# Performance work log

Hardware: AMD Instinct MI355X
Metric: run time of the kernel (lower is better)

Reference implementation:

```python
import jax, jax.numpy as jnp
import numpy as np

N_QUBITS = 8
N_LAYERS = 2
BATCH = 16384
DIM = 2 ** N_QUBITS

# PauliZ sign table: Z[q, idx] = +1 if bit q of idx is 0 else -1 (qubit 0 = MSB,
# matching state axis ordering below).
_bits = (np.arange(DIM)[:, None] >> (N_QUBITS - 1 - np.arange(N_QUBITS))) & 1
Z_SIGNS = jnp.asarray((1 - 2 * _bits).T.astype(np.float32))  # (n_qubits, 2^n)


def _apply_1q(state, gates, q):
    """Apply batched single-qubit gate. state: (B,)+(2,)*n complex, gates: (B,2,2)."""
    s = jnp.moveaxis(state, 1 + q, -1)
    s = jnp.einsum('nab,...b->...a', gates, s.reshape(gates.shape[0], -1, 2).reshape(s.shape))
    # the einsum above: gates (B,2,2) broadcast over the intermediate axes
    return jnp.moveaxis(s, -1, 1 + q)


def _apply_1q_batched(state, gates, q):
    s = jnp.moveaxis(state, 1 + q, -1)          # (B, ..., 2)
    s = jnp.einsum('nab,n...b->n...a', gates, s)
    return jnp.moveaxis(s, -1, 1 + q)


def _apply_cnot(state, c, t):
    s = jnp.moveaxis(state, (1 + c, 1 + t), (-2, -1))  # (..., 2_ctrl, 2_tgt)
    s = jnp.concatenate([s[..., :1, :], s[..., 1:, ::-1]], axis=-2)  # flip target where ctrl=1
    return jnp.moveaxis(s, (-2, -1), (1 + c, 1 + t))


def _rx_gate(theta):
    """Batched RX(theta): (B,) -> (B,2,2) complex."""
    c = jnp.cos(theta / 2)
    s = -1j * jnp.sin(theta / 2)
    return jnp.stack([jnp.stack([c + 0j, s], -1), jnp.stack([s, c + 0j], -1)], -2)


def _rot_gate(phi, theta, omega):
    """PennyLane Rot(phi,theta,omega) = RZ(omega) RY(theta) RZ(phi). Batched (B,)->(B,2,2)."""
    c = jnp.cos(theta / 2)
    s = jnp.sin(theta / 2)
    ep = jnp.exp(-0.5j * (phi + omega))  # e^{-i(phi+omega)/2}
    em = jnp.exp(0.5j * (phi - omega))   # e^{ i(phi-omega)/2}
    m00 = ep * c
    m01 = -em * s
    m10 = jnp.conj(em) * s
    m11 = jnp.conj(ep) * c
    return jnp.stack([jnp.stack([m00, m01], -1), jnp.stack([m10, m11], -1)], -2)


def _circuit(inputs, hidden):
    B = inputs.shape[0]
    n = N_QUBITS
    state = jnp.zeros((B,) + (2,) * n, jnp.complex64)
    state = state.at[(slice(None),) + (0,) * n].set(1.0 + 0j)
    # AngleEmbedding: RX(inputs[:, q]) on each wire q
    for q in range(n):
        state = _apply_1q_batched(state, _rx_gate(inputs[:, q]), q)
    # n_layers calls of StronglyEntanglingLayers, each with 1 layer of weights
    for l in range(N_LAYERS):
        w = hidden[:, l, 0]  # (B, n_qubits, 3)
        for q in range(n):
            state = _apply_1q_batched(state, _rot_gate(w[:, q, 0], w[:, q, 1], w[:, q, 2]), q)
        for q in range(n):  # CNOT ring, range r = 1
            state = _apply_cnot(state, q, (q + 1) % n)
    probs = jnp.abs(state.reshape(B, DIM)) ** 2          # (B, 2^n)
    expvals = probs @ Z_SIGNS.T                          # (B, n_qubits) <Z_q>
    return jnp.tanh(expvals)


def setup_inputs() -> dict:
    key = jax.random.key(0)
    k1, k2 = jax.random.split(key)
    inputs = jax.random.normal(k1, (BATCH, N_QUBITS), dtype=jnp.float32)
    hidden = jax.random.normal(k2, (BATCH, N_LAYERS, 1, N_QUBITS, 3), dtype=jnp.float32)
    return {"inputs": inputs, "hidden": hidden}


def reference(inputs, hidden):
    h = _circuit(inputs, hidden)
    return (h, h)
```

## Files before the change

### kernel.cpp

```cpp
#include <hip/hip_runtime.h>
#include <math.h>


#define DEVINL __device__ __forceinline__

DEVINL void fast_sincos_half(float x, float& s, float& c) {
    const float r = x * 0.07957747154594767f;
    s = __builtin_amdgcn_sinf(r);
    c = __builtin_amdgcn_cosf(r);
}

DEVINL float fast_tanh(float x) {
    const float t = __builtin_amdgcn_exp2f(x * 2.8853900817779268f);
    return 1.0f - 2.0f * __builtin_amdgcn_rcpf(t + 1.0f);
}

DEVINL void cmul(float ar, float ai, float br, float bi, float& cr, float& ci) {
    cr = ar*br - ai*bi;
    ci = ar*bi + ai*br;
}

template<int CTRL>
DEVINL float dpp_perm(float x) {
    return __int_as_float(__builtin_amdgcn_update_dpp(
        __float_as_int(x), __float_as_int(x), CTRL, 0xF, 0xF, false));
}

DEVINL void qubit_vec(float x, float phi, float theta, float omega,
                      float& v0r, float& v0i, float& v1r, float& v1i)
{
    float s, c;   fast_sincos_half(x, s, c);
    float st, ct; fast_sincos_half(theta, st, ct);
    float sa, ca; fast_sincos_half(phi + omega, sa, ca);
    float sb, cb; fast_sincos_half(phi - omega, sb, cb);
    const float A = c*ct, B = s*st, C = c*st, D = s*ct;
    v0r = ca*A - sb*B;
    v0i = cb*B - sa*A;
    v1r = cb*C + sa*D;
    v1i = -(sb*C + ca*D);
}

template<int KM>
DEVINL void ry_k(float (&ar)[16], float (&ai)[16], float c, float s) {
    #pragma unroll
    for (int k0 = 0; k0 < 16; ++k0) {
        if (k0 & KM) continue;
        const int k1 = k0 | KM;
        const float lr = ar[k0], li = ai[k0], hr = ar[k1], hi = ai[k1];
        ar[k0] = c*lr - s*hr;  ai[k0] = c*li - s*hi;
        ar[k1] = s*lr + c*hr;  ai[k1] = s*li + c*hi;
    }
}

template<int CTRL>
DEVINL void ry_lane(float (&ar)[16], float (&ai)[16], float c, float seff) {
    #pragma unroll
    for (int k = 0; k < 16; ++k) {
        const float pr = dpp_perm<CTRL>(ar[k]);
        const float pi = dpp_perm<CTRL>(ai[k]);
        ar[k] = c*ar[k] + seff*pr;
        ai[k] = c*ai[k] + seff*pi;
    }
}

__global__ __launch_bounds__(256, 4)
void qcirc_kernel(const float* __restrict__ inputs,
                  const float* __restrict__ hidden,
                  float* __restrict__ out, int B)
{
    const int t  = threadIdx.x;
    const int e  = blockIdx.x * 16 + (t >> 4);
    const int sl = t & 15;
    if (e >= B) return;

    const int sl0 = sl & 1, sl1 = (sl >> 1) & 1, sl2 = (sl >> 2) & 1, sl3 = (sl >> 3) & 1;
    const int p01 = sl0 ^ sl1;

    float inv[8], hv[48];
    {
        const float4* ip = (const float4*)(inputs + (size_t)e * 8);
        ((float4*)inv)[0] = ip[0];
        ((float4*)inv)[1] = ip[1];
        const float4* hp = (const float4*)(hidden + (size_t)e * 48);
        #pragma unroll
        for (int j = 0; j < 12; ++j) ((float4*)hv)[j] = hp[j];
    }

    float vr[8][2], vi[8][2];
    #pragma unroll
    for (int q = 0; q < 8; ++q)
        qubit_vec(inv[q], hv[q*3], hv[q*3+1], hv[q*3+2],
                  vr[q][0], vi[q][0], vr[q][1], vi[q][1]);

    const float w0r0 = p01 ? vr[0][1] : vr[0][0], w0i0 = p01 ? vi[0][1] : vi[0][0];
    const float w0r1 = p01 ? vr[0][0] : vr[0][1], w0i1 = p01 ? vi[0][0] : vi[0][1];
    const float w1r0 = p01 ? vr[1][1] : vr[1][0], w1i0 = p01 ? vi[1][1] : vi[1][0];
    const float w1r1 = p01 ? vr[1][0] : vr[1][1], w1i1 = p01 ? vi[1][0] : vi[1][1];
    const float w4r0 = sl3 ? vr[4][1] : vr[4][0], w4i0 = sl3 ? vi[4][1] : vi[4][0];
    const float w4r1 = sl3 ? vr[4][0] : vr[4][1], w4i1 = sl3 ? vi[4][0] : vi[4][1];

    float Lr, Li;
    {
        const int s6 = sl1 ^ sl3, s7 = sl0 ^ sl2;
        const float ar5 = sl2 ? vr[5][1] : vr[5][0], ai5 = sl2 ? vi[5][1] : vi[5][0];
        const float ar6 = s6  ? vr[6][1] : vr[6][0], ai6 = s6  ? vi[6][1] : vi[6][0];
        const float ar7 = s7  ? vr[7][1] : vr[7][0], ai7 = s7  ? vi[7][1] : vi[7][0];
        float tr, ti;
        cmul(ar5, ai5, ar6, ai6, tr, ti);
        cmul(tr, ti, ar7, ai7, Lr, Li);
    }

    float KAr[4], KAi[4];
    #pragma unroll
    for (int j = 0; j < 4; ++j) {
        const int k3 = j >> 1, k2 = j & 1, x = k3 ^ k2;
        const float f0r = k3 ? w0r1 : w0r0, f0i = k3 ? w0i1 : w0i0;
        const float f1r = x  ? w1r1 : w1r0, f1i = x  ? w1i1 : w1i0;
        float tr, ti;
        cmul(f0r, f0i, f1r, f1i, tr, ti);
        cmul(tr, ti, Lr, Li, KAr[j], KAi[j]);
    }
    float KCr[4], KCi[4];
    #pragma unroll
    for (int m = 0; m < 4; ++m) {
        const int k1 = m >> 1, k0 = m & 1, x = k0 ^ k1;
        const float f4r = k0 ? w4r1 : w4r0, f4i = k0 ? w4i1 : w4i0;
        cmul(vr[3][x], vi[3][x], f4r, f4i, KCr[m], KCi[m]);
    }
    float K8r[8], K8i[8];
    #pragma unroll
    for (int m = 0; m < 8; ++m) {
        const int k2 = m >> 2, k1 = (m >> 1) & 1, x = k1 ^ k2;
        cmul(vr[2][x], vi[2][x], KCr[m & 3], KCi[m & 3], K8r[m], K8i[m]);
    }

    const float REV2 = 0.07957747154594767f;
    float h[8];
    #pragma unroll
    for (int p = 0; p < 8; ++p) h[p] = hv[24 + p*3] * REV2;
    const float lam = (sl3        ? h[4] : -h[4]) + ((sl3^sl2) ? h[5] : -h[5])
                    + ((sl2^sl1)  ? h[6] : -h[6]) + ((sl1^sl0) ? h[7] : -h[7]);
    float Aang[4];
    Aang[0] = lam - h[0] - h[1];
    Aang[1] = lam - h[0] + h[1];
    Aang[2] = lam + h[0] - h[1];
    Aang[3] = lam + h[0] + h[1];
    const float Bs = h[2] + h[3], Bd = h[2] - h[3];

    float ar[16], ai[16];
    #pragma unroll
    for (int k = 0; k < 16; ++k) {
        const int j = k >> 2, m = k & 7, mm = k & 3;
        const float ang = Aang[j] + (mm == 0 ? -Bs : mm == 1 ? -Bd : mm == 2 ? Bd : Bs);
        const float cr = __builtin_amdgcn_cosf(ang);
        const float ci = __builtin_amdgcn_sinf(ang);
        float tr, ti;
        cmul(KAr[j], KAi[j], K8r[m], K8i[m], tr, ti);
        cmul(tr, ti, cr, ci, ar[k], ai[k]);
    }

    float s2[8], c2[8];
    #pragma unroll
    for (int p = 0; p < 8; ++p) fast_sincos_half(hv[24 + p*3 + 1], s2[p], c2[p]);

    ry_k<8>(ar, ai, c2[0], s2[0]);
    ry_k<4>(ar, ai, c2[1], s2[1]);
    ry_k<2>(ar, ai, c2[2], s2[2]);
    ry_k<1>(ar, ai, c2[3], s2[3]);

    const float e4 = sl3        ? s2[4] : -s2[4];
    const float e5 = (sl3^sl2)  ? s2[5] : -s2[5];
    const float e6 = (sl2^sl1)  ? s2[6] : -s2[6];
    const float e7 = (sl1^sl0)  ? s2[7] : -s2[7];
    ry_lane<0x140>(ar, ai, c2[4], e4);
    ry_lane<0x141>(ar, ai, c2[5], e5);
    ry_lane<0x1B> (ar, ai, c2[6], e6);
    ry_lane<0xB1> (ar, ai, c2[7], e7);

    float P[16];
    #pragma unroll
    for (int k = 0; k < 16; ++k) P[k] = ar[k]*ar[k] + ai[k]*ai[k];

    float S0[4], S1[4], S3[4];
    #pragma unroll
    for (int j = 0; j < 4; ++j) {
        const float p00 = P[j*4+0], p01v = P[j*4+1], p10 = P[j*4+2], p11 = P[j*4+3];
        const float u = p00 + p01v, w = p10 + p11;
        const float d0 = p00 - p01v, d1 = p10 - p11;
        S0[j] = u + w;
        S1[j] = u - w;
        S3[j] = d0 - d1;
    }
    float VC = S0[0] - S0[1] - S0[2] + S0[3];
    float VE = S1[0] - S1[1] - S1[2] + S1[3];
    float VF = S3[0] - S3[1] - S3[2] + S3[3];
    float V7 = S3[0] - S3[1] + S3[2] - S3[3];

    {
        const float g1 = (sl & 1) ? -1.f : 1.f;
        V7 = fmaf(g1, V7, dpp_perm<0xB1>(V7));
        VC = fmaf(g1, VC, dpp_perm<0xB1>(VC));
        VE = fmaf(g1, VE, dpp_perm<0xB1>(VE));
        VF = fmaf(g1, VF, dpp_perm<0xB1>(VF));
        const float g2 = (sl & 2) ? -1.f : 1.f;
        V7 = fmaf(g2, V7, dpp_perm<0x4E>(V7));
        VC = fmaf(g2, VC, dpp_perm<0x4E>(VC));
        VE = fmaf(g2, VE, dpp_perm<0x4E>(VE));
        VF = fmaf(g2, VF, dpp_perm<0x4E>(VF));
        const float g4 = (sl & 4) ? -1.f : 1.f;
        V7 = fmaf(g4, V7, __shfl_xor(V7, 4, 64));
        VC = fmaf(g4, VC, __shfl_xor(VC, 4, 64));
        VE = fmaf(g4, VE, __shfl_xor(VE, 4, 64));
        VF = fmaf(g4, VF, __shfl_xor(VF, 4, 64));
        const float g8 = (sl & 8) ? -1.f : 1.f;
        V7 = fmaf(g8, V7, __shfl_xor(V7, 8, 64));
        VC = fmaf(g8, VC, __shfl_xor(VC, 8, 64));
        VE = fmaf(g8, VE, __shfl_xor(VE, 8, 64));
        VF = fmaf(g8, VF, __shfl_xor(VF, 8, 64));
    }

    const int gb = (t & 63) & 48;
    const float B7 = __shfl(V7, gb + 1, 64);
    const float BC = __shfl(VC, gb, 64);
    const float BE = __shfl(VE, gb, 64);
    const int fidx = (sl >= 4) ? (128 >> sl) : 0;
    const float BF = __shfl(VF, gb + fidx, 64);
    const float rsel = (sl == 0) ? B7 : (sl == 1) ? BC : (sl == 2) ? BE : BF;
    const float hres = fast_tanh(rsel);
    if (sl < 8) {
        const size_t obase = (size_t)e * 8;
        const size_t half  = (size_t)B * 8;
        out[obase + sl]        = hres;
        out[half + obase + sl] = hres;
    }
}

extern "C" void kernel_launch(void* const* d_in, const int* in_sizes, int n_in,
                              void* d_out, int out_size, void* d_ws, size_t ws_size,
                              hipStream_t stream)
{
    const float* inputs = (const float*)d_in[0];
    const float* hidden = (const float*)d_in[1];
    float* out = (float*)d_out;
    const int B = in_sizes[0] / 8;
    const int blocks = (B + 15) / 16;
    hipLaunchKernelGGL(qcirc_kernel, dim3(blocks), dim3(256), 0, stream,
                       inputs, hidden, out, B);
}
```

Before: 15.67 us.

## Split each circuit across 32 lanes with 8 amplitudes per lane

Each batch element's 256-amplitude state now spans 32 lanes holding 8 amplitudes each, instead of 16 lanes holding 16. Per-qubit trig setup is spread so each lane computes one qubit's vector and angles, then the values are passed between lanes by shuffle rather than every lane recomputing all eight. The phase factors are folded algebraically so fewer sin/cos calls are needed per amplitude. This lowers register pressure (launch bounds raised to 8) and redundant work, at the cost of more cross-lane shuffles, including xor-16 shuffles through LDS, and twice as many threads per element.

```diff
diff --git a/kernel.cpp b/kernel.cpp
--- a/kernel.cpp
+++ b/kernel.cpp
@@ -18,6 +18,10 @@
 DEVINL void cmul(float ar, float ai, float br, float bi, float& cr, float& ci) {
     cr = ar*br - ai*bi;
     ci = ar*bi + ai*br;
+}
+DEVINL void cmulc(float ar, float ai, float br, float bi, float& cr, float& ci) {
+    cr = ar*br + ai*bi;
+    ci = ar*bi - ai*br;
 }
 
 template<int CTRL>
@@ -41,9 +45,9 @@
 }
 
 template<int KM>
-DEVINL void ry_k(float (&ar)[16], float (&ai)[16], float c, float s) {
-    #pragma unroll
-    for (int k0 = 0; k0 < 16; ++k0) {
+DEVINL void ry_k8(float (&ar)[8], float (&ai)[8], float c, float s) {
+    #pragma unroll
+    for (int k0 = 0; k0 < 8; ++k0) {
         if (k0 & KM) continue;
         const int k1 = k0 | KM;
         const float lr = ar[k0], li = ai[k0], hr = ar[k1], hi = ai[k1];
@@ -53,9 +57,9 @@
 }
 
 template<int CTRL>
-DEVINL void ry_lane(float (&ar)[16], float (&ai)[16], float c, float seff) {
-    #pragma unroll
-    for (int k = 0; k < 16; ++k) {
+DEVINL void ry_lane8(float (&ar)[8], float (&ai)[8], float c, float seff) {
+    #pragma unroll
+    for (int k = 0; k < 8; ++k) {
         const float pr = dpp_perm<CTRL>(ar[k]);
         const float pi = dpp_perm<CTRL>(ai[k]);
         ar[k] = c*ar[k] + seff*pr;
@@ -63,175 +67,194 @@
     }
 }
 
-__global__ __launch_bounds__(256, 4)
+DEVINL void ry_xor16(float (&ar)[8], float (&ai)[8], float c, float seff) {
+    #pragma unroll
+    for (int k = 0; k < 8; ++k) {
+        const float pr = __shfl_xor(ar[k], 16, 64);
+        const float pi = __shfl_xor(ai[k], 16, 64);
+        ar[k] = c*ar[k] + seff*pr;
+        ai[k] = c*ai[k] + seff*pi;
+    }
+}
+
+__global__ __launch_bounds__(256, 8)
 void qcirc_kernel(const float* __restrict__ inputs,
                   const float* __restrict__ hidden,
                   float* __restrict__ out, int B)
 {
     const int t  = threadIdx.x;
-    const int e  = blockIdx.x * 16 + (t >> 4);
-    const int sl = t & 15;
+    const int e  = blockIdx.x * 8 + (t >> 5);
     if (e >= B) return;
-
-    const int sl0 = sl & 1, sl1 = (sl >> 1) & 1, sl2 = (sl >> 2) & 1, sl3 = (sl >> 3) & 1;
-    const int p01 = sl0 ^ sl1;
-
-    float inv[8], hv[48];
-    {
-        const float4* ip = (const float4*)(inputs + (size_t)e * 8);
-        ((float4*)inv)[0] = ip[0];
-        ((float4*)inv)[1] = ip[1];
-        const float4* hp = (const float4*)(hidden + (size_t)e * 48);
+    const int sl = t & 31;
+    const int gb = t & 32;
+    const int q  = sl & 7;
+    const int sl0 = sl & 1, sl1 = (sl >> 1) & 1, sl2 = (sl >> 2) & 1,
+              sl3 = (sl >> 3) & 1, sl4 = (sl >> 4) & 1;
+
+    const float  x   = inputs[(size_t)e * 8 + q];
+    const float* hb  = hidden + (size_t)e * 48 + q * 3;
+    const float ph1 = hb[0], th1 = hb[1], om1 = hb[2];
+    const float ph2 = hb[24], th2 = hb[25];
+
+    float ov0r, ov0i, ov1r, ov1i;
+    qubit_vec(x, ph1, th1, om1, ov0r, ov0i, ov1r, ov1i);
+    float s2o, c2o; fast_sincos_half(th2, s2o, c2o);
+    const float ho  = ph2 * 0.07957747154594767f;
+    const float Eco = __builtin_amdgcn_cosf(ho);
+    const float Eso = __builtin_amdgcn_sinf(ho);
+
+    float Lr, Li;
+    {
+        float fr[4][2], fi[4][2];
         #pragma unroll
-        for (int j = 0; j < 12; ++j) ((float4*)hv)[j] = hp[j];
-    }
-
-    float vr[8][2], vi[8][2];
-    #pragma unroll
-    for (int q = 0; q < 8; ++q)
-        qubit_vec(inv[q], hv[q*3], hv[q*3+1], hv[q*3+2],
-                  vr[q][0], vi[q][0], vr[q][1], vi[q][1]);
-
-    const float w0r0 = p01 ? vr[0][1] : vr[0][0], w0i0 = p01 ? vi[0][1] : vi[0][0];
-    const float w0r1 = p01 ? vr[0][0] : vr[0][1], w0i1 = p01 ? vi[0][0] : vi[0][1];
-    const float w1r0 = p01 ? vr[1][1] : vr[1][0], w1i0 = p01 ? vi[1][1] : vi[1][0];
-    const float w1r1 = p01 ? vr[1][0] : vr[1][1], w1i1 = p01 ? vi[1][0] : vi[1][1];
-    const float w4r0 = sl3 ? vr[4][1] : vr[4][0], w4i0 = sl3 ? vi[4][1] : vi[4][0];
-    const float w4r1 = sl3 ? vr[4][0] : vr[4][1], w4i1 = sl3 ? vi[4][0] : vi[4][1];
-
-    float Lr, Li;
-    {
-        const int s6 = sl1 ^ sl3, s7 = sl0 ^ sl2;
-        const float ar5 = sl2 ? vr[5][1] : vr[5][0], ai5 = sl2 ? vi[5][1] : vi[5][0];
-        const float ar6 = s6  ? vr[6][1] : vr[6][0], ai6 = s6  ? vi[6][1] : vi[6][0];
-        const float ar7 = s7  ? vr[7][1] : vr[7][0], ai7 = s7  ? vi[7][1] : vi[7][0];
+        for (int p = 0; p < 4; ++p) {
+            fr[p][0] = __shfl(ov0r, gb + 4 + p, 64);
+            fi[p][0] = __shfl(ov0i, gb + 4 + p, 64);
+            fr[p][1] = __shfl(ov1r, gb + 4 + p, 64);
+            fi[p][1] = __shfl(ov1i, gb + 4 + p, 64);
+        }
+        const int s4 = sl3 ^ sl4, s5 = sl2 ^ sl3, s6 = sl1, s7 = sl0 ^ sl1;
+        const float a4r = s4 ? fr[0][1] : fr[0][0], a4i = s4 ? fi[0][1] : fi[0][0];
+        const float a5r = s5 ? fr[1][1] : fr[1][0], a5i = s5 ? fi[1][1] : fi[1][0];
+        const float a6r = s6 ? fr[2][1] : fr[2][0], a6i = s6 ? fi[2][1] : fi[2][0];
+        const float a7r = s7 ? fr[3][1] : fr[3][0], a7i = s7 ? fi[3][1] : fi[3][0];
         float tr, ti;
-        cmul(ar5, ai5, ar6, ai6, tr, ti);
-        cmul(tr, ti, ar7, ai7, Lr, Li);
-    }
-
-    float KAr[4], KAi[4];
-    #pragma unroll
-    for (int j = 0; j < 4; ++j) {
-        const int k3 = j >> 1, k2 = j & 1, x = k3 ^ k2;
-        const float f0r = k3 ? w0r1 : w0r0, f0i = k3 ? w0i1 : w0i0;
-        const float f1r = x  ? w1r1 : w1r0, f1i = x  ? w1i1 : w1i0;
+        cmul(a4r, a4i, a5r, a5i, tr, ti);
+        cmul(tr, ti, a6r, a6i, Lr, Li);
+        cmul(Lr, Li, a7r, a7i, tr, ti);
+        Lr = tr; Li = ti;
+    }
+
+    const float E0c = __shfl(Eco, gb + 0, 64), E0s = __shfl(Eso, gb + 0, 64);
+    const float E1c = __shfl(Eco, gb + 1, 64), E1s = __shfl(Eso, gb + 1, 64);
+    const float E2c = __shfl(Eco, gb + 2, 64), E2s = __shfl(Eso, gb + 2, 64);
+    {
+        const float h3 = __shfl(ho, gb + 3, 64);
+        const float h4 = __shfl(ho, gb + 4, 64);
+        const float h5 = __shfl(ho, gb + 5, 64);
+        const float h6 = __shfl(ho, gb + 6, 64);
+        const float h7 = __shfl(ho, gb + 7, 64);
+        const float lam = (sl4 ? h3 : -h3) + (sl3 ? h4 : -h4) + (sl2 ? h5 : -h5)
+                        + ((sl1 ^ sl2) ? h6 : -h6) + ((sl0 ^ sl2) ? h7 : -h7);
+        const float Pc = __builtin_amdgcn_cosf(lam);
+        const float Ps = __builtin_amdgcn_sinf(lam);
+        float tr, ti; cmul(Lr, Li, Pc, Ps, tr, ti);
+        Lr = tr; Li = ti;
+    }
+
+    float vr[4][2], vi[4][2];
+    #pragma unroll
+    for (int p = 0; p < 4; ++p) {
+        vr[p][0] = __shfl(ov0r, gb + p, 64);
+        vi[p][0] = __shfl(ov0i, gb + p, 64);
+        vr[p][1] = __shfl(ov1r, gb + p, 64);
+        vi[p][1] = __shfl(ov1i, gb + p, 64);
+    }
+
+    const int b01 = sl0 ^ sl2;
+    const float w0r0 = b01 ? vr[0][1] : vr[0][0], w0i0 = b01 ? vi[0][1] : vi[0][0];
+    const float w0r1 = b01 ? vr[0][0] : vr[0][1], w0i1 = b01 ? vi[0][0] : vi[0][1];
+    const float w1r0 = b01 ? vr[1][1] : vr[1][0], w1i0 = b01 ? vi[1][1] : vi[1][0];
+    const float w1r1 = b01 ? vr[1][0] : vr[1][1], w1i1 = b01 ? vi[1][0] : vi[1][1];
+    const float w3r0 = sl4 ? vr[3][1] : vr[3][0], w3i0 = sl4 ? vi[3][1] : vi[3][0];
+    const float w3r1 = sl4 ? vr[3][0] : vr[3][1], w3i1 = sl4 ? vi[3][0] : vi[3][1];
+
+    float w3p0r, w3p0i, w3p1r, w3p1i;
+    cmulc(E2c, E2s, w3r0, w3i0, w3p0r, w3p0i);
+    cmul (w3r1, w3i1, E2c, E2s, w3p1r, w3p1i);
+
+    float GL0r, GL0i, GL1r, GL1i, GL2r, GL2i, GL3r, GL3i;
+    {
+        const float a = E0c*E1c, b = E0s*E1s, c = E0c*E1s, d = E0s*E1c;
+        const float P3r = a - b, P3i = c + d;
+        const float P1r = a + b, P1i = c - d;
+        cmulc(P3r, P3i, Lr, Li, GL0r, GL0i);
+        cmul (P1r, P1i, Lr, Li, GL1r, GL1i);
+        cmulc(P1r, P1i, Lr, Li, GL2r, GL2i);
+        cmul (P3r, P3i, Lr, Li, GL3r, GL3i);
+    }
+
+    float T2r[4], T2i[4], T1r[4], T1i[4];
+    {
         float tr, ti;
-        cmul(f0r, f0i, f1r, f1i, tr, ti);
-        cmul(tr, ti, Lr, Li, KAr[j], KAi[j]);
-    }
-    float KCr[4], KCi[4];
-    #pragma unroll
-    for (int m = 0; m < 4; ++m) {
-        const int k1 = m >> 1, k0 = m & 1, x = k0 ^ k1;
-        const float f4r = k0 ? w4r1 : w4r0, f4i = k0 ? w4i1 : w4i0;
-        cmul(vr[3][x], vi[3][x], f4r, f4i, KCr[m], KCi[m]);
-    }
-    float K8r[8], K8i[8];
-    #pragma unroll
-    for (int m = 0; m < 8; ++m) {
-        const int k2 = m >> 2, k1 = (m >> 1) & 1, x = k1 ^ k2;
-        cmul(vr[2][x], vi[2][x], KCr[m & 3], KCi[m & 3], K8r[m], K8i[m]);
-    }
-
-    const float REV2 = 0.07957747154594767f;
-    float h[8];
-    #pragma unroll
-    for (int p = 0; p < 8; ++p) h[p] = hv[24 + p*3] * REV2;
-    const float lam = (sl3        ? h[4] : -h[4]) + ((sl3^sl2) ? h[5] : -h[5])
-                    + ((sl2^sl1)  ? h[6] : -h[6]) + ((sl1^sl0) ? h[7] : -h[7]);
-    float Aang[4];
-    Aang[0] = lam - h[0] - h[1];
-    Aang[1] = lam - h[0] + h[1];
-    Aang[2] = lam + h[0] - h[1];
-    Aang[3] = lam + h[0] + h[1];
-    const float Bs = h[2] + h[3], Bd = h[2] - h[3];
-
-    float ar[16], ai[16];
-    #pragma unroll
-    for (int k = 0; k < 16; ++k) {
-        const int j = k >> 2, m = k & 7, mm = k & 3;
-        const float ang = Aang[j] + (mm == 0 ? -Bs : mm == 1 ? -Bd : mm == 2 ? Bd : Bs);
-        const float cr = __builtin_amdgcn_cosf(ang);
-        const float ci = __builtin_amdgcn_sinf(ang);
-        float tr, ti;
-        cmul(KAr[j], KAi[j], K8r[m], K8i[m], tr, ti);
-        cmul(tr, ti, cr, ci, ar[k], ai[k]);
-    }
-
-    float s2[8], c2[8];
-    #pragma unroll
-    for (int p = 0; p < 8; ++p) fast_sincos_half(hv[24 + p*3 + 1], s2[p], c2[p]);
-
-    ry_k<8>(ar, ai, c2[0], s2[0]);
-    ry_k<4>(ar, ai, c2[1], s2[1]);
-    ry_k<2>(ar, ai, c2[2], s2[2]);
-    ry_k<1>(ar, ai, c2[3], s2[3]);
-
-    const float e4 = sl3        ? s2[4] : -s2[4];
-    const float e5 = (sl3^sl2)  ? s2[5] : -s2[5];
-    const float e6 = (sl2^sl1)  ? s2[6] : -s2[6];
-    const float e7 = (sl1^sl0)  ? s2[7] : -s2[7];
-    ry_lane<0x140>(ar, ai, c2[4], e4);
-    ry_lane<0x141>(ar, ai, c2[5], e5);
-    ry_lane<0x1B> (ar, ai, c2[6], e6);
-    ry_lane<0xB1> (ar, ai, c2[7], e7);
-
-    float P[16];
-    #pragma unroll
-    for (int k = 0; k < 16; ++k) P[k] = ar[k]*ar[k] + ai[k]*ai[k];
-
-    float S0[4], S1[4], S3[4];
-    #pragma unroll
-    for (int j = 0; j < 4; ++j) {
-        const float p00 = P[j*4+0], p01v = P[j*4+1], p10 = P[j*4+2], p11 = P[j*4+3];
-        const float u = p00 + p01v, w = p10 + p11;
-        const float d0 = p00 - p01v, d1 = p10 - p11;
-        S0[j] = u + w;
-        S1[j] = u - w;
-        S3[j] = d0 - d1;
-    }
-    float VC = S0[0] - S0[1] - S0[2] + S0[3];
-    float VE = S1[0] - S1[1] - S1[2] + S1[3];
-    float VF = S3[0] - S3[1] - S3[2] + S3[3];
-    float V7 = S3[0] - S3[1] + S3[2] - S3[3];
+        cmul(w0r0, w0i0, w1r0, w1i0, tr, ti); cmul(tr, ti, GL0r, GL0i, T2r[0], T2i[0]);
+        cmul(w0r0, w0i0, w1r1, w1i1, tr, ti); cmul(tr, ti, GL1r, GL1i, T2r[1], T2i[1]);
+        cmul(w0r1, w0i1, w1r1, w1i1, tr, ti); cmul(tr, ti, GL2r, GL2i, T2r[2], T2i[2]);
+        cmul(w0r1, w0i1, w1r0, w1i0, tr, ti); cmul(tr, ti, GL3r, GL3i, T2r[3], T2i[3]);
+        cmul(vr[2][0], vi[2][0], w3p0r, w3p0i, T1r[0], T1i[0]);
+        cmul(vr[2][1], vi[2][1], w3p1r, w3p1i, T1r[1], T1i[1]);
+        cmul(vr[2][1], vi[2][1], w3p0r, w3p0i, T1r[2], T1i[2]);
+        cmul(vr[2][0], vi[2][0], w3p1r, w3p1i, T1r[3], T1i[3]);
+    }
+
+    float ar[8], ai[8];
+    #pragma unroll
+    for (int k = 0; k < 8; ++k) {
+        cmul(T2r[k >> 1], T2i[k >> 1], T1r[k & 3], T1i[k & 3], ar[k], ai[k]);
+    }
+
+    { const float c = __shfl(c2o, gb + 0, 64), s = __shfl(s2o, gb + 0, 64);
+      ry_k8<4>(ar, ai, c, s); }
+    { const float c = __shfl(c2o, gb + 1, 64), s = __shfl(s2o, gb + 1, 64);
+      ry_k8<2>(ar, ai, c, s); }
+    { const float c = __shfl(c2o, gb + 2, 64), s = __shfl(s2o, gb + 2, 64);
+      ry_k8<1>(ar, ai, c, s); }
+    { const float c = __shfl(c2o, gb + 3, 64), s = __shfl(s2o, gb + 3, 64);
+      ry_xor16(ar, ai, c, sl4 ? s : -s); }
+    { const float c = __shfl(c2o, gb + 4, 64), s = __shfl(s2o, gb + 4, 64);
+      ry_lane8<0x128>(ar, ai, c, sl3 ? s : -s); }
+    { const float c = __shfl(c2o, gb + 5, 64), s = __shfl(s2o, gb + 5, 64);
+      ry_lane8<0x141>(ar, ai, c, sl2 ? s : -s); }
+    { const float c = __shfl(c2o, gb + 6, 64), s = __shfl(s2o, gb + 6, 64);
+      ry_lane8<0x4E>(ar, ai, c, (sl1 ^ sl2) ? s : -s); }
+    { const float c = __shfl(c2o, gb + 7, 64), s = __shfl(s2o, gb + 7, 64);
+      ry_lane8<0xB1>(ar, ai, c, (sl0 ^ sl2) ? s : -s); }
+
+    float P[8];
+    #pragma unroll
+    for (int k = 0; k < 8; ++k) P[k] = ar[k]*ar[k] + ai[k]*ai[k];
+    const float u0 = P[0]+P[1], v0 = P[0]-P[1];
+    const float u1 = P[2]+P[3], v1 = P[2]-P[3];
+    const float u2 = P[4]+P[5], v2 = P[4]-P[5];
+    const float u3 = P[6]+P[7], v3 = P[6]-P[7];
+    float V3 = v0 - v1 + v2 - v3;
+    float V6 = u0 - u1 - u2 + u3;
+    float V7 = v0 - v1 - v2 + v3;
 
     {
         const float g1 = (sl & 1) ? -1.f : 1.f;
+        V3 = fmaf(g1, V3, dpp_perm<0xB1>(V3));
+        V6 = fmaf(g1, V6, dpp_perm<0xB1>(V6));
         V7 = fmaf(g1, V7, dpp_perm<0xB1>(V7));
-        VC = fmaf(g1, VC, dpp_perm<0xB1>(VC));
-        VE = fmaf(g1, VE, dpp_perm<0xB1>(VE));
-        VF = fmaf(g1, VF, dpp_perm<0xB1>(VF));
         const float g2 = (sl & 2) ? -1.f : 1.f;
+        V3 = fmaf(g2, V3, dpp_perm<0x4E>(V3));
+        V6 = fmaf(g2, V6, dpp_perm<0x4E>(V6));
         V7 = fmaf(g2, V7, dpp_perm<0x4E>(V7));
-        VC = fmaf(g2, VC, dpp_perm<0x4E>(VC));
-        VE = fmaf(g2, VE, dpp_perm<0x4E>(VE));
-        VF = fmaf(g2, VF, dpp_perm<0x4E>(VF));
         const float g4 = (sl & 4) ? -1.f : 1.f;
+        V3 = fmaf(g4, V3, __shfl_xor(V3, 4, 64));
+        V6 = fmaf(g4, V6, __shfl_xor(V6, 4, 64));
         V7 = fmaf(g4, V7, __shfl_xor(V7, 4, 64));
-        VC = fmaf(g4, VC, __shfl_xor(VC, 4, 64));
-        VE = fmaf(g4, VE, __shfl_xor(VE, 4, 64));
-        VF = fmaf(g4, VF, __shfl_xor(VF, 4, 64));
         const float g8 = (sl & 8) ? -1.f : 1.f;
-        V7 = fmaf(g8, V7, __shfl_xor(V7, 8, 64));
-        VC = fmaf(g8, VC, __shfl_xor(VC, 8, 64));
-        VE = fmaf(g8, VE, __shfl_xor(VE, 8, 64));
-        VF = fmaf(g8, VF, __shfl_xor(VF, 8, 64));
-    }
-
-    const int gb = (t & 63) & 48;
-    const float B7 = __shfl(V7, gb + 1, 64);
-    const float BC = __shfl(VC, gb, 64);
-    const float BE = __shfl(VE, gb, 64);
-    const int fidx = (sl >= 4) ? (128 >> sl) : 0;
-    const float BF = __shfl(VF, gb + fidx, 64);
-    const float rsel = (sl == 0) ? B7 : (sl == 1) ? BC : (sl == 2) ? BE : BF;
-    const float hres = fast_tanh(rsel);
+        V3 = fmaf(g8, V3, dpp_perm<0x128>(V3));
+        V6 = fmaf(g8, V6, dpp_perm<0x128>(V6));
+        V7 = fmaf(g8, V7, dpp_perm<0x128>(V7));
+        const float g16 = (sl & 16) ? -1.f : 1.f;
+        V3 = fmaf(g16, V3, __shfl_xor(V3, 16, 64));
+        V6 = fmaf(g16, V6, __shfl_xor(V6, 16, 64));
+        V7 = fmaf(g16, V7, __shfl_xor(V7, 16, 64));
+    }
+
+    const int idx7 = (sl == 3) ? 16 : (sl == 4) ? 24 : (sl == 5) ? 28
+                   : (sl == 6) ? 26 : (sl == 7) ? 31 : 0;
+    const float B3 = __shfl(V3, gb + 31, 64);
+    const float B6 = __shfl(V6, gb + 0, 64);
+    const float B7 = __shfl(V7, gb + idx7, 64);
+    const float rsel = (sl == 0) ? B3 : (sl == 1) ? B6 : B7;
+    const float h = fast_tanh(rsel);
     if (sl < 8) {
         const size_t obase = (size_t)e * 8;
-        const size_t half  = (size_t)B * 8;
-        out[obase + sl]        = hres;
-        out[half + obase + sl] = hres;
+        out[obase + sl] = h;
+        out[(size_t)B * 8 + obase + sl] = h;
     }
 }
 
@@ -243,7 +266,7 @@
     const float* hidden = (const float*)d_in[1];
     float* out = (float*)d_out;
     const int B = in_sizes[0] / 8;
-    const int blocks = (B + 15) / 16;
+    const int blocks = (B + 7) / 8;
     hipLaunchKernelGGL(qcirc_kernel, dim3(blocks), dim3(256), 0, stream,
                        inputs, hidden, out, B);
 }
```

Result: faster. 14.93 us (-4.7%).
